# Kernel optimization log

Measured on AMD Instinct MI355X. Metric: run time of the kernel, lower is better.

The kernel has to match this reference:

```python
import jax, jax.numpy as jnp
import numpy as np

LEAK = 0.01
TEMP = 1.0
N_ORB = 1024
CTX = 32
N_ALPHA = 32
N_BETA = 32
B = 8192
EPS = 1e-20


def _leaky(x):
    return jnp.where(x >= 0, x, LEAK * x)


def _scorer_mlp(x, W1, b1, W2, b2, W3, b3):
    h = _leaky(x @ W1 + b1)
    h = _leaky(h @ W2 + b2)
    return h @ W3 + b3


def _gumbel_topk(logits, gumbel, k, temp):
    # successive-softmax subset relaxation (Plackett-Luce style)
    scores0 = logits + gumbel

    def step(carry, _):
        scores, khot = carry
        onehot = jax.nn.softmax(scores / temp, axis=-1)
        khot = khot + onehot
        scores = scores + jnp.log(jnp.maximum(1.0 - onehot, EPS))
        return (scores, khot), None

    (_, khot), _ = jax.lax.scan(step, (scores0, jnp.zeros_like(scores0)), None, length=k)
    return khot


def _soft_to_hard(soft, k):
    # straight-through: hard forward, soft backward
    idx = jax.lax.top_k(soft, k)[1]                      # (B, k)
    bidx = jnp.arange(soft.shape[0])[:, None]
    hard = jnp.zeros_like(soft).at[bidx, idx].set(1.0)
    return jax.lax.stop_gradient(hard - soft) + soft


def _lin_init(key, fan_in, fan_out):
    s = 1.0 / np.sqrt(fan_in)
    k1, k2 = jax.random.split(key)
    W = jax.random.uniform(k1, (fan_in, fan_out), minval=-s, maxval=s, dtype=jnp.float32)
    b = jax.random.uniform(k2, (fan_out,), minval=-s, maxval=s, dtype=jnp.float32)
    return W, b


def setup_inputs() -> dict:
    key = jax.random.key(0)
    ks = jax.random.split(key, 12)
    # alpha scorer: input = n_orb (baseline only, context_dim=0)
    W1a, b1a = _lin_init(ks[0], N_ORB, 128)
    W2a, b2a = _lin_init(ks[1], 128, 64)
    W3a, b3a = _lin_init(ks[2], 64, N_ORB)
    # beta scorer: context proj n_orb -> 32, input = n_orb + 32
    Wc, bc = _lin_init(ks[3], N_ORB, CTX)
    W1b, b1b = _lin_init(ks[4], N_ORB + CTX, 128)
    W2b, b2b = _lin_init(ks[5], 128, 64)
    W3b, b3b = _lin_init(ks[6], 64, N_ORB)
    baseline_a = jnp.zeros((N_ORB,), jnp.float32)
    baseline_b = jnp.zeros((N_ORB,), jnp.float32)
    # Gumbel noise: -log(-log(U))
    ua = jax.random.uniform(ks[7], (B, N_ORB), minval=1e-6, maxval=1.0 - 1e-6)
    ub = jax.random.uniform(ks[8], (B, N_ORB), minval=1e-6, maxval=1.0 - 1e-6)
    g_alpha = -jnp.log(-jnp.log(ua))
    g_beta = -jnp.log(-jnp.log(ub))
    return {
        "baseline_a": baseline_a, "W1a": W1a, "b1a": b1a, "W2a": W2a, "b2a": b2a,
        "W3a": W3a, "b3a": b3a,
        "baseline_b": baseline_b, "Wc": Wc, "bc": bc, "W1b": W1b, "b1b": b1b,
        "W2b": W2b, "b2b": b2b, "W3b": W3b, "b3b": b3b,
        "g_alpha": g_alpha, "g_beta": g_beta,
        "batch_size": B,
    }


def reference(baseline_a, W1a, b1a, W2a, b2a, W3a, b3a,
              baseline_b, Wc, bc, W1b, b1b, W2b, b2b, W3b, b3b,
              g_alpha, g_beta, batch_size):
    # --- alpha scoring (context_dim = 0) ---
    base_a = jnp.broadcast_to(baseline_a, (batch_size, N_ORB))
    alpha_logits = _scorer_mlp(base_a, W1a, b1a, W2a, b2a, W3a, b3a) + base_a
    alpha_soft = _gumbel_topk(alpha_logits, g_alpha, N_ALPHA, TEMP)
    alpha_config = _soft_to_hard(alpha_soft, N_ALPHA)          # (B, N_ORB)
    # --- beta scoring conditioned on alpha config ---
    base_b = jnp.broadcast_to(baseline_b, (batch_size, N_ORB))
    ctx = alpha_config @ Wc + bc                               # (B, 32)
    net_in = jnp.concatenate([base_b, ctx], axis=-1)
    beta_logits = _scorer_mlp(net_in, W1b, b1b, W2b, b2b, W3b, b3b) + base_b
    beta_soft = _gumbel_topk(beta_logits, g_beta, N_BETA, TEMP)
    beta_config = _soft_to_hard(beta_soft, N_BETA)
    return jnp.concatenate([alpha_config, beta_config], axis=-1)  # (B, num_sites)
```

## Files before the change

kernel.cpp:

```cpp
#include <hip/hip_runtime.h>
#include <hip/hip_bf16.h>
#include <float.h>

#define N_ORB 1024
#define KSEL 32
#define LEAK 0.01f

typedef float f32x2 __attribute__((ext_vector_type(2)));

__device__ __forceinline__ float leaky(float x) { return x >= 0.0f ? x : LEAK * x; }

__device__ __forceinline__ unsigned fkey(float f) {
  const unsigned u = __float_as_uint(f);
  return u ^ ((unsigned)((int)u >> 31) | 0x80000000u);
}

template <int CTRL, int RM>
__device__ __forceinline__ int dpp0_i(int v) {
  return __builtin_amdgcn_update_dpp(0, v, CTRL, RM, 0xF, true);
}
template <int CTRL>
__device__ __forceinline__ float dpp_zero(float v) {
  return __int_as_float(
      __builtin_amdgcn_update_dpp(0, __float_as_int(v), CTRL, 0xF, 0xF, true));
}
__device__ __forceinline__ float rdlane(float v, int l) {
  return __int_as_float(__builtin_amdgcn_readlane(__float_as_int(v), l));
}

__device__ __forceinline__ float wave_sum64_dpp(float v) {
  v += dpp_zero<0x111>(v);
  v += dpp_zero<0x112>(v);
  v += dpp_zero<0x114>(v);
  v += dpp_zero<0x118>(v);
  v += dpp_zero<0x142>(v);
  v += dpp_zero<0x143>(v);
  return rdlane(v, 63);
}
__device__ __forceinline__ int wave_isum64(int v) {
  v += dpp0_i<0x111, 0xF>(v);
  v += dpp0_i<0x112, 0xF>(v);
  v += dpp0_i<0x114, 0xF>(v);
  v += dpp0_i<0x118, 0xF>(v);
  v += dpp0_i<0x142, 0xF>(v);
  v += dpp0_i<0x143, 0xF>(v);
  return __builtin_amdgcn_readlane(v, 63);
}
__device__ __forceinline__ int wave_iscan64(int v) {
  v += dpp0_i<0x111, 0xF>(v);
  v += dpp0_i<0x112, 0xF>(v);
  v += dpp0_i<0x114, 0xF>(v);
  v += dpp0_i<0x118, 0xF>(v);
  v += dpp0_i<0x142, 0xA>(v);
  v += dpp0_i<0x143, 0xC>(v);
  return v;
}

__device__ unsigned tie_mask16u(const unsigned K[16], unsigned T, int lane) {
  unsigned gt = 0, eq = 0;
#pragma unroll
  for (int i = 0; i < 16; ++i) {
    gt |= (K[i] > T ? 1u : 0u) << i;
    eq |= (K[i] == T ? 1u : 0u) << i;
  }
  const int n_gt = wave_isum64(__popc(gt));
  const int m = 32 - n_gt;
  const int pe = __popc(eq);
  const int be = wave_iscan64(pe) - pe;
  int need = m - be;
  need = need < 0 ? 0 : (need > pe ? pe : need);
  unsigned tk = 0;
  unsigned em = eq;
  for (int guard = 0; guard < 16; ++guard) {
    if (!__any(need > 0)) break;
    if (need > 0) {
      const int bpos = __ffs(em) - 1;
      tk |= 1u << bpos;
      em &= em - 1;
      --need;
    }
  }
  return gt | tk;
}

__device__ void top32_mask2u(const unsigned K0[16], const unsigned K1[16],
                             int lane, unsigned& m0, unsigned& m1) {
  unsigned lo0 = 0, lo1 = 0;
  bool ex0 = false, ex1 = false;
  for (int b = 31; b >= 0; --b) {
    const unsigned c0v = lo0 | (1u << b);
    const unsigned c1v = lo1 | (1u << b);
    int c0 = 0, c1 = 0;
#pragma unroll
    for (int i = 0; i < 16; ++i) {
      c0 += __popcll(__ballot(K0[i] >= c0v));
      c1 += __popcll(__ballot(K1[i] >= c1v));
    }
    if (!ex0 && c0 >= 32) { lo0 = c0v; ex0 = (c0 == 32); }
    if (!ex1 && c1 >= 32) { lo1 = c1v; ex1 = (c1 == 32); }
    if (ex0 && ex1) break;
  }

  if (ex0) {
    unsigned mk = 0;
#pragma unroll
    for (int i = 0; i < 16; ++i) mk |= (K0[i] >= lo0 ? 1u : 0u) << i;
    m0 = mk;
  } else {
    m0 = tie_mask16u(K0, lo0, lane);
  }
  if (ex1) {
    unsigned mk = 0;
#pragma unroll
    for (int i = 0; i < 16; ++i) mk |= (K1[i] >= lo1 ? 1u : 0u) << i;
    m1 = mk;
  } else {
    m1 = tie_mask16u(K1, lo1, lane);
  }
}

__device__ __forceinline__ void compact_idx(unsigned mask, int lane,
                                            int* __restrict__ dst) {
  const int pe = __popc(mask);
  int base = wave_iscan64(pe) - pe;
  unsigned m = mask;
  while (m) {
    const int s = __ffs(m) - 1;
    m &= m - 1;
    dst[base++] = (lane << 4) | s;
  }
}

__device__ __forceinline__ void write_half(float* __restrict__ dst,
                                           unsigned mask, int lane) {
  float4* o4 = (float4*)dst;
#pragma unroll
  for (int q = 0; q < 4; ++q) {
    float4 o;
    o.x = ((mask >> (4 * q + 0)) & 1) ? 1.0f : 0.0f;
    o.y = ((mask >> (4 * q + 1)) & 1) ? 1.0f : 0.0f;
    o.z = ((mask >> (4 * q + 2)) & 1) ? 1.0f : 0.0f;
    o.w = ((mask >> (4 * q + 3)) & 1) ? 1.0f : 0.0f;
    o4[lane * 4 + q] = o;
  }
}


extern "C" __global__ void pcfs_pre1(const float* __restrict__ ba,
                                     const float* __restrict__ W1a,
                                     const float* __restrict__ b1a,
                                     const float* __restrict__ bb,
                                     const float* __restrict__ W1b,
                                     float* __restrict__ ws) {
  const int b = blockIdx.x;
  const int t = threadIdx.x;
  float acc = 0.0f;
  if (b < 128) {
#pragma unroll
    for (int j = t; j < N_ORB; j += 256) acc += ba[j] * W1a[j * 128 + b];
  } else {
    const int n = b - 128;
#pragma unroll
    for (int j = t; j < N_ORB; j += 256) acc += bb[j] * W1b[j * 128 + n];
  }
  __shared__ float red[4];
  float wsum = wave_sum64_dpp(acc);
  if ((t & 63) == 0) red[t >> 6] = wsum;
  __syncthreads();
  if (t == 0) {
    float tot = red[0] + red[1] + red[2] + red[3];
    if (b < 128)
      ws[1152 + b] = leaky(tot + b1a[b]);
    else
      ws[N_ORB + (b - 128)] = tot;
  }
}

extern "C" __global__ void pcfs_pre2a(const float* __restrict__ W2a,
                                      const float* __restrict__ b2a,
                                      float* __restrict__ ws) {
  const int t = threadIdx.x;
  float acc = b2a[t];
#pragma unroll 8
  for (int n = 0; n < 128; ++n) acc = __builtin_fmaf(ws[1152 + n], W2a[n * 64 + t], acc);
  ws[1280 + t] = leaky(acc);
}

extern "C" __global__ void pcfs_pre2b(const float* __restrict__ ba,
                                      const float* __restrict__ W3a,
                                      const float* __restrict__ b3a,
                                      float* __restrict__ ws) {
  __shared__ float h2s[64];
  const int t = threadIdx.x;
  const int o = blockIdx.x * 256 + t;
  if (t < 64) h2s[t] = ws[1280 + t];
  __syncthreads();
  float acc = b3a[o] + ba[o];
#pragma unroll 8
  for (int m = 0; m < 64; ++m) acc = __builtin_fmaf(h2s[m], W3a[m * N_ORB + o], acc);
  ws[o] = acc;
}

extern "C" __global__ void __launch_bounds__(256, 4) pcfs_sampler(
    const float* __restrict__ ws, const float* __restrict__ Wc,
    const float* __restrict__ bc, const float* __restrict__ W1b,
    const float* __restrict__ b1b, const float* __restrict__ W2b,
    const float* __restrict__ b2b, const float* __restrict__ W3b,
    const float* __restrict__ b3b, const float* __restrict__ bb,
    const float* __restrict__ g_alpha, const float* __restrict__ g_beta,
    float* __restrict__ out, int B) {
  __shared__ int sidx[4][64];
  __shared__ float w3s[8 * N_ORB];
  const int tid = threadIdx.x;
  const int wave = tid >> 6;
  const int lane = tid & 63;
  const int pair = blockIdx.x * 4 + wave;
  const int row0 = pair * 2;
  const bool active = (row0 < B);
  const bool have1 = active && (row0 + 1 < B);
  const int r0 = active ? row0 : 0;
  const int r1 = have1 ? row0 + 1 : r0;

  float4 gb0[4], gb1[4];
  {
    const float4* g40 = (const float4*)(g_beta + (size_t)r0 * N_ORB);
    const float4* g41 = (const float4*)(g_beta + (size_t)r1 * N_ORB);
#pragma unroll
    for (int q = 0; q < 4; ++q) {
      gb0[q] = g40[lane * 4 + q];
      gb1[q] = g41[lane * 4 + q];
    }
  }

  unsigned ka0[16], ka1[16];
  {
    const float4* c4 = (const float4*)ws;
    const float4* g40 = (const float4*)(g_alpha + (size_t)r0 * N_ORB);
    const float4* g41 = (const float4*)(g_alpha + (size_t)r1 * N_ORB);
#pragma unroll
    for (int q = 0; q < 4; ++q) {
      float4 c = c4[lane * 4 + q];
      float4 g0 = g40[lane * 4 + q];
      float4 g1 = g41[lane * 4 + q];
      ka0[4 * q + 0] = fkey(c.x + g0.x); ka1[4 * q + 0] = fkey(c.x + g1.x);
      ka0[4 * q + 1] = fkey(c.y + g0.y); ka1[4 * q + 1] = fkey(c.y + g1.y);
      ka0[4 * q + 2] = fkey(c.z + g0.z); ka1[4 * q + 2] = fkey(c.z + g1.z);
      ka0[4 * q + 3] = fkey(c.w + g0.w); ka1[4 * q + 3] = fkey(c.w + g1.w);
    }
  }
  unsigned am0, am1;
  top32_mask2u(ka0, ka1, lane, am0, am1);

  if (active) write_half(out + (size_t)row0 * (2 * N_ORB), am0, lane);
  if (have1) write_half(out + (size_t)(row0 + 1) * (2 * N_ORB), am1, lane);

  compact_idx(am0, lane, &sidx[wave][0]);
  compact_idx(am1, lane, &sidx[wave][32]);
  const int vi0 = sidx[wave][lane & 31];
  const int vi1 = sidx[wave][32 + (lane & 31)];
  const float bcv = bc[lane & 31];
  float ctx0 = bcv, ctx1 = bcv;
#pragma unroll
  for (int r = 0; r < 32; ++r) {
    const int i0 = __builtin_amdgcn_readlane(vi0, r);
    const int i1 = __builtin_amdgcn_readlane(vi1, r);
    ctx0 += Wc[i0 * 32 + (lane & 31)];
    ctx1 += Wc[i1 * 32 + (lane & 31)];
  }

  f32x2 h1a, h1b_;
  {
    const float ia = b1b[lane] + ws[N_ORB + lane];
    const float ib = b1b[lane + 64] + ws[N_ORB + lane + 64];
    h1a = f32x2{ia, ia};
    h1b_ = f32x2{ib, ib};
  }
#pragma unroll 4
  for (int c = 0; c < 32; ++c) {
    const f32x2 cv = f32x2{rdlane(ctx0, c), rdlane(ctx1, c)};
    const float* wr = W1b + (size_t)(N_ORB + c) * 128;
    const float wa = wr[lane], wb = wr[lane + 64];
    h1a = __builtin_elementwise_fma(f32x2{wa, wa}, cv, h1a);
    h1b_ = __builtin_elementwise_fma(f32x2{wb, wb}, cv, h1b_);
  }
  h1a = f32x2{leaky(h1a.x), leaky(h1a.y)};
  h1b_ = f32x2{leaky(h1b_.x), leaky(h1b_.y)};

  f32x2 h2p0, h2p1, h2p2, h2p3;
  {
    const float i2 = b2b[lane];
    h2p0 = f32x2{i2, i2};
    h2p1 = f32x2{0.0f, 0.0f};
    h2p2 = f32x2{0.0f, 0.0f};
    h2p3 = f32x2{0.0f, 0.0f};
  }
#pragma unroll 4
  for (int n = 0; n < 64; n += 4) {
    const f32x2 v0 = f32x2{rdlane(h1a.x, n + 0), rdlane(h1a.y, n + 0)};
    const f32x2 v1 = f32x2{rdlane(h1a.x, n + 1), rdlane(h1a.y, n + 1)};
    const f32x2 v2 = f32x2{rdlane(h1a.x, n + 2), rdlane(h1a.y, n + 2)};
    const f32x2 v3 = f32x2{rdlane(h1a.x, n + 3), rdlane(h1a.y, n + 3)};
    const float w0 = W2b[(n + 0) * 64 + lane];
    const float w1 = W2b[(n + 1) * 64 + lane];
    const float w2 = W2b[(n + 2) * 64 + lane];
    const float w3 = W2b[(n + 3) * 64 + lane];
    h2p0 = __builtin_elementwise_fma(f32x2{w0, w0}, v0, h2p0);
    h2p1 = __builtin_elementwise_fma(f32x2{w1, w1}, v1, h2p1);
    h2p2 = __builtin_elementwise_fma(f32x2{w2, w2}, v2, h2p2);
    h2p3 = __builtin_elementwise_fma(f32x2{w3, w3}, v3, h2p3);
  }
#pragma unroll 4
  for (int n = 0; n < 64; n += 4) {
    const f32x2 v0 = f32x2{rdlane(h1b_.x, n + 0), rdlane(h1b_.y, n + 0)};
    const f32x2 v1 = f32x2{rdlane(h1b_.x, n + 1), rdlane(h1b_.y, n + 1)};
    const f32x2 v2 = f32x2{rdlane(h1b_.x, n + 2), rdlane(h1b_.y, n + 2)};
    const f32x2 v3 = f32x2{rdlane(h1b_.x, n + 3), rdlane(h1b_.y, n + 3)};
    const float w0 = W2b[(n + 64 + 0) * 64 + lane];
    const float w1 = W2b[(n + 64 + 1) * 64 + lane];
    const float w2 = W2b[(n + 64 + 2) * 64 + lane];
    const float w3 = W2b[(n + 64 + 3) * 64 + lane];
    h2p0 = __builtin_elementwise_fma(f32x2{w0, w0}, v0, h2p0);
    h2p1 = __builtin_elementwise_fma(f32x2{w1, w1}, v1, h2p1);
    h2p2 = __builtin_elementwise_fma(f32x2{w2, w2}, v2, h2p2);
    h2p3 = __builtin_elementwise_fma(f32x2{w3, w3}, v3, h2p3);
  }
  f32x2 h2v = (h2p0 + h2p1) + (h2p2 + h2p3);
  h2v = f32x2{leaky(h2v.x), leaky(h2v.y)};

  f32x2 w[16];
  {
    const float4* b4 = (const float4*)b3b;
#pragma unroll
    for (int q = 0; q < 4; ++q) {
      float4 b = b4[lane * 4 + q];
      w[4 * q + 0] = f32x2{b.x, b.x};
      w[4 * q + 1] = f32x2{b.y, b.y};
      w[4 * q + 2] = f32x2{b.z, b.z};
      w[4 * q + 3] = f32x2{b.w, b.w};
    }
  }
  const int swzrd = ((lane & 1) << 7) | (lane >> 1);
  const int swzwr = ((tid & 7) << 5) | (tid >> 3);
  for (int t = 0; t < 8; ++t) {
    __syncthreads();
    {
      const float4* src = (const float4*)(W3b + (size_t)t * 8 * N_ORB);
      float4* dst = (float4*)w3s;
#pragma unroll
      for (int k = 0; k < 8; ++k) dst[k * 256 + swzwr] = src[tid + k * 256];
    }
    __syncthreads();
#pragma unroll
    for (int ml = 0; ml < 8; ++ml) {
      const int m = t * 8 + ml;
      const f32x2 hm = f32x2{rdlane(h2v.x, m), rdlane(h2v.y, m)};
      const float4* w4 = (const float4*)(w3s + ml * N_ORB);
#pragma unroll
      for (int q = 0; q < 4; ++q) {
        float4 wv = w4[swzrd + (q << 5)];
        w[4 * q + 0] = __builtin_elementwise_fma(f32x2{wv.x, wv.x}, hm, w[4 * q + 0]);
        w[4 * q + 1] = __builtin_elementwise_fma(f32x2{wv.y, wv.y}, hm, w[4 * q + 1]);
        w[4 * q + 2] = __builtin_elementwise_fma(f32x2{wv.z, wv.z}, hm, w[4 * q + 2]);
        w[4 * q + 3] = __builtin_elementwise_fma(f32x2{wv.w, wv.w}, hm, w[4 * q + 3]);
      }
    }
  }
  unsigned kb0[16], kb1[16];
  {
    const float4* bb4 = (const float4*)bb;
#pragma unroll
    for (int q = 0; q < 4; ++q) {
      float4 b = bb4[lane * 4 + q];
      const float4 g0 = gb0[q];
      const float4 g1 = gb1[q];
      kb0[4 * q + 0] = fkey(w[4 * q + 0].x + b.x + g0.x);
      kb1[4 * q + 0] = fkey(w[4 * q + 0].y + b.x + g1.x);
      kb0[4 * q + 1] = fkey(w[4 * q + 1].x + b.y + g0.y);
      kb1[4 * q + 1] = fkey(w[4 * q + 1].y + b.y + g1.y);
      kb0[4 * q + 2] = fkey(w[4 * q + 2].x + b.z + g0.z);
      kb1[4 * q + 2] = fkey(w[4 * q + 2].y + b.z + g1.z);
      kb0[4 * q + 3] = fkey(w[4 * q + 3].x + b.w + g0.w);
      kb1[4 * q + 3] = fkey(w[4 * q + 3].y + b.w + g1.w);
    }
  }
  unsigned bm0, bm1;
  top32_mask2u(kb0, kb1, lane, bm0, bm1);

  if (active) write_half(out + (size_t)row0 * (2 * N_ORB) + N_ORB, bm0, lane);
  if (have1)
    write_half(out + (size_t)(row0 + 1) * (2 * N_ORB) + N_ORB, bm1, lane);
}

extern "C" void kernel_launch(void* const* d_in, const int* in_sizes, int n_in,
                              void* d_out, int out_size, void* d_ws, size_t ws_size,
                              hipStream_t stream) {
  const float* ba  = (const float*)d_in[0];
  const float* W1a = (const float*)d_in[1];
  const float* b1a = (const float*)d_in[2];
  const float* W2a = (const float*)d_in[3];
  const float* b2a = (const float*)d_in[4];
  const float* W3a = (const float*)d_in[5];
  const float* b3a = (const float*)d_in[6];
  const float* bb  = (const float*)d_in[7];
  const float* Wc  = (const float*)d_in[8];
  const float* bc  = (const float*)d_in[9];
  const float* W1b = (const float*)d_in[10];
  const float* b1b = (const float*)d_in[11];
  const float* W2b = (const float*)d_in[12];
  const float* b2b = (const float*)d_in[13];
  const float* W3b = (const float*)d_in[14];
  const float* b3b = (const float*)d_in[15];
  const float* ga  = (const float*)d_in[16];
  const float* gbt = (const float*)d_in[17];
  const int B = in_sizes[16] / N_ORB;
  float* ws = (float*)d_ws;

  hipLaunchKernelGGL(pcfs_pre1, dim3(256), dim3(256), 0, stream,
                     ba, W1a, b1a, bb, W1b, ws);
  hipLaunchKernelGGL(pcfs_pre2a, dim3(1), dim3(64), 0, stream,
                     W2a, b2a, ws);
  hipLaunchKernelGGL(pcfs_pre2b, dim3(4), dim3(256), 0, stream,
                     ba, W3a, b3a, ws);
  const int pairs = (B + 1) / 2;
  hipLaunchKernelGGL(pcfs_sampler, dim3((pairs + 3) / 4), dim3(256), 0, stream,
                     ws, Wc, bc, W1b, b1b, W2b, b2b, W3b, b3b, bb,
                     ga, gbt, (float*)d_out, B);
}
```

Before: 240.5 us.

## Compute W3b layer block-cooperatively with per-wave column slices and LDS logit exchange

The third beta-MLP layer used to stage W3b through shared memory in eight tiles with barriers, and each wave computed all 1024 outputs for its two rows. Now the block shares all eight rows' hidden vectors via LDS. Each wave reads its own 256-column slice of W3b straight from global memory and accumulates for all eight rows with packed FMA through inline asm. Results go to an LDS logits buffer and are redistributed back to each wave's row layout. This removes the repeated LDS staging and barrier loop and reuses each W3b load across eight rows, at the cost of an extra LDS round trip and more accumulator registers.

Result: faster. 229.8 us, median of 2 (-4.4%).

```diff
diff --git a/kernel.cpp b/kernel.cpp
--- a/kernel.cpp
+++ b/kernel.cpp
@@ -13,6 +13,12 @@
 __device__ __forceinline__ unsigned fkey(float f) {
   const unsigned u = __float_as_uint(f);
   return u ^ ((unsigned)((int)u >> 31) | 0x80000000u);
+}
+
+__device__ __forceinline__ f32x2 pk_fma(f32x2 a, f32x2 b, f32x2 c) {
+  f32x2 d;
+  asm("v_pk_fma_f32 %0, %1, %2, %3" : "=v"(d) : "v"(a), "v"(b), "v"(c));
+  return d;
 }
 
 template <int CTRL, int RM>
@@ -210,7 +216,8 @@
     const float* __restrict__ g_alpha, const float* __restrict__ g_beta,
     float* __restrict__ out, int B) {
   __shared__ int sidx[4][64];
-  __shared__ float w3s[8 * N_ORB];
+  __shared__ float lgt[8 * N_ORB];
+  __shared__ f32x2 h2sh[4 * 64];
   const int tid = threadIdx.x;
   const int wave = tid >> 6;
   const int lane = tid & 63;
@@ -327,42 +334,74 @@
   f32x2 h2v = (h2p0 + h2p1) + (h2p2 + h2p3);
   h2v = f32x2{leaky(h2v.x), leaky(h2v.y)};
 
+  h2sh[wave * 64 + lane] = h2v;
+  __syncthreads();
+  f32x2 hh0 = h2sh[0 * 64 + lane];
+  f32x2 hh1 = h2sh[1 * 64 + lane];
+  f32x2 hh2 = h2sh[2 * 64 + lane];
+  f32x2 hh3 = h2sh[3 * 64 + lane];
+
+  const int cbase = wave * 64 + lane;
+  f32x2 acc[4][4];
+  {
+    const float4 b3v = ((const float4*)b3b)[cbase];
+#pragma unroll
+    for (int rp = 0; rp < 4; ++rp) {
+      acc[rp][0] = f32x2{b3v.x, b3v.x};
+      acc[rp][1] = f32x2{b3v.y, b3v.y};
+      acc[rp][2] = f32x2{b3v.z, b3v.z};
+      acc[rp][3] = f32x2{b3v.w, b3v.w};
+    }
+  }
+  {
+    const float4* w34 = (const float4*)W3b;
+#pragma unroll 4
+    for (int m = 0; m < 64; ++m) {
+      const float4 wv = w34[(m << 8) + cbase];
+      const f32x2 h0 = f32x2{rdlane(hh0.x, m), rdlane(hh0.y, m)};
+      const f32x2 h1 = f32x2{rdlane(hh1.x, m), rdlane(hh1.y, m)};
+      const f32x2 h2_ = f32x2{rdlane(hh2.x, m), rdlane(hh2.y, m)};
+      const f32x2 h3 = f32x2{rdlane(hh3.x, m), rdlane(hh3.y, m)};
+      acc[0][0] = pk_fma(f32x2{wv.x, wv.x}, h0, acc[0][0]);
+      acc[0][1] = pk_fma(f32x2{wv.y, wv.y}, h0, acc[0][1]);
+      acc[0][2] = pk_fma(f32x2{wv.z, wv.z}, h0, acc[0][2]);
+      acc[0][3] = pk_fma(f32x2{wv.w, wv.w}, h0, acc[0][3]);
+      acc[1][0] = pk_fma(f32x2{wv.x, wv.x}, h1, acc[1][0]);
+      acc[1][1] = pk_fma(f32x2{wv.y, wv.y}, h1, acc[1][1]);
+      acc[1][2] = pk_fma(f32x2{wv.z, wv.z}, h1, acc[1][2]);
+      acc[1][3] = pk_fma(f32x2{wv.w, wv.w}, h1, acc[1][3]);
+      acc[2][0] = pk_fma(f32x2{wv.x, wv.x}, h2_, acc[2][0]);
+      acc[2][1] = pk_fma(f32x2{wv.y, wv.y}, h2_, acc[2][1]);
+      acc[2][2] = pk_fma(f32x2{wv.z, wv.z}, h2_, acc[2][2]);
+      acc[2][3] = pk_fma(f32x2{wv.w, wv.w}, h2_, acc[2][3]);
+      acc[3][0] = pk_fma(f32x2{wv.x, wv.x}, h3, acc[3][0]);
+      acc[3][1] = pk_fma(f32x2{wv.y, wv.y}, h3, acc[3][1]);
+      acc[3][2] = pk_fma(f32x2{wv.z, wv.z}, h3, acc[3][2]);
+      acc[3][3] = pk_fma(f32x2{wv.w, wv.w}, h3, acc[3][3]);
+    }
+  }
+#pragma unroll
+  for (int rp = 0; rp < 4; ++rp) {
+    float4 ex, ey;
+    ex.x = acc[rp][0].x; ex.y = acc[rp][1].x; ex.z = acc[rp][2].x; ex.w = acc[rp][3].x;
+    ey.x = acc[rp][0].y; ey.y = acc[rp][1].y; ey.z = acc[rp][2].y; ey.w = acc[rp][3].y;
+    ((float4*)(lgt + (2 * rp) * N_ORB))[cbase] = ex;
+    ((float4*)(lgt + (2 * rp + 1) * N_ORB))[cbase] = ey;
+  }
+  __syncthreads();
+
   f32x2 w[16];
   {
-    const float4* b4 = (const float4*)b3b;
+    const float4* lr0 = (const float4*)(lgt + (2 * wave) * N_ORB);
+    const float4* lr1 = (const float4*)(lgt + (2 * wave + 1) * N_ORB);
 #pragma unroll
     for (int q = 0; q < 4; ++q) {
-      float4 b = b4[lane * 4 + q];
-      w[4 * q + 0] = f32x2{b.x, b.x};
-      w[4 * q + 1] = f32x2{b.y, b.y};
-      w[4 * q + 2] = f32x2{b.z, b.z};
-      w[4 * q + 3] = f32x2{b.w, b.w};
-    }
-  }
-  const int swzrd = ((lane & 1) << 7) | (lane >> 1);
-  const int swzwr = ((tid & 7) << 5) | (tid >> 3);
-  for (int t = 0; t < 8; ++t) {
-    __syncthreads();
-    {
-      const float4* src = (const float4*)(W3b + (size_t)t * 8 * N_ORB);
-      float4* dst = (float4*)w3s;
-#pragma unroll
-      for (int k = 0; k < 8; ++k) dst[k * 256 + swzwr] = src[tid + k * 256];
-    }
-    __syncthreads();
-#pragma unroll
-    for (int ml = 0; ml < 8; ++ml) {
-      const int m = t * 8 + ml;
-      const f32x2 hm = f32x2{rdlane(h2v.x, m), rdlane(h2v.y, m)};
-      const float4* w4 = (const float4*)(w3s + ml * N_ORB);
-#pragma unroll
-      for (int q = 0; q < 4; ++q) {
-        float4 wv = w4[swzrd + (q << 5)];
-        w[4 * q + 0] = __builtin_elementwise_fma(f32x2{wv.x, wv.x}, hm, w[4 * q + 0]);
-        w[4 * q + 1] = __builtin_elementwise_fma(f32x2{wv.y, wv.y}, hm, w[4 * q + 1]);
-        w[4 * q + 2] = __builtin_elementwise_fma(f32x2{wv.z, wv.z}, hm, w[4 * q + 2]);
-        w[4 * q + 3] = __builtin_elementwise_fma(f32x2{wv.w, wv.w}, hm, w[4 * q + 3]);
-      }
+      const float4 a = lr0[lane * 4 + q];
+      const float4 b = lr1[lane * 4 + q];
+      w[4 * q + 0] = f32x2{a.x, b.x};
+      w[4 * q + 1] = f32x2{a.y, b.y};
+      w[4 * q + 2] = f32x2{a.z, b.z};
+      w[4 * q + 3] = f32x2{a.w, b.w};
     }
   }
   unsigned kb0[16], kb1[16];
```
